# Optimization experiments

Measured on AMD Instinct MI355X. Metric: run time of the kernel, lower is better.

The kernel has to match this reference:

```python
import jax, jax.numpy as jnp
import numpy as np

B, S, D_IN, H, SD = 512, 1024, 64, 64, 4


def setup_inputs() -> dict:
    key = jax.random.key(0)
    ks = jax.random.split(key, 12)
    sc_in = 1.0 / np.sqrt(D_IN)
    sc_h = 1.0 / np.sqrt(H)
    sc_c = 1.0 / np.sqrt(SD + H)
    return {
        "x": jax.random.normal(ks[0], (B, S, D_IN), jnp.float32),
        "W1": jax.random.uniform(ks[1], (H, D_IN), jnp.float32, -sc_in, sc_in),
        "b1": jax.random.uniform(ks[2], (H,), jnp.float32, -sc_in, sc_in),
        "ln_g": jnp.ones((H,), jnp.float32),
        "ln_b": jnp.zeros((H,), jnp.float32),
        "Wi": jax.random.uniform(ks[3], (SD, H), jnp.float32, -sc_h, sc_h),
        "bi": jax.random.uniform(ks[4], (SD,), jnp.float32, -sc_h, sc_h),
        "Wc1": jax.random.uniform(ks[5], (H, SD + H), jnp.float32, -sc_c, sc_c),
        "bc1": jax.random.uniform(ks[6], (H,), jnp.float32, -sc_c, sc_c),
        "Wc2": jax.random.uniform(ks[7], (SD, H), jnp.float32, -sc_h, sc_h),
        "bc2": jax.random.uniform(ks[8], (SD,), jnp.float32, -sc_h, sc_h),
        "corr_scale": jnp.asarray(0.01, jnp.float32),
        "A_level": jnp.zeros((1,), jnp.float32),
        "A_trend": jnp.zeros((1,), jnp.float32),
        "A_gamma": jnp.zeros((1,), jnp.float32),
        "A_resid": jnp.zeros((1,), jnp.float32),
        "omega": jnp.zeros((1,), jnp.float32),
    }


def reference(x, W1, b1, ln_g, ln_b, Wi, bi, Wc1, bc1, Wc2, bc2,
              corr_scale, A_level, A_trend, A_gamma, A_resid, omega):
    # input_proj: Linear -> LayerNorm -> GELU (exact erf), dropout=0
    h = jnp.einsum('bsd,hd->bsh', x, W1) + b1
    mu = jnp.mean(h, axis=-1, keepdims=True)
    var = jnp.mean((h - mu) ** 2, axis=-1, keepdims=True)
    h = (h - mu) * jax.lax.rsqrt(var + 1e-5) * ln_g + ln_b
    h = jax.nn.gelu(h, approximate=False)  # [B,S,H]

    # structured A for state_dim == 4: diag(a_l, a_t, gamma*cos(w), a_r)
    a_l = jax.nn.sigmoid(A_level) * 0.15 + 0.85
    a_t = jax.nn.sigmoid(A_trend) * 0.25 + 0.7
    gamma = jax.nn.sigmoid(A_gamma) * 0.2 + 0.8
    a_r = jax.nn.sigmoid(A_resid) * 0.4
    A = jnp.diag(jnp.concatenate([a_l, a_t, gamma * jnp.cos(omega), a_r]))  # [4,4]

    # innovation applied to all steps at once (batched tiny GEMM)
    bx = jnp.einsum('bsh,kh->bsk', h, Wi) + bi  # [B,S,4]

    def step(s, inp):
        bx_t, h_t = inp  # [B,4], [B,H]
        s_lin = s @ A.T + bx_t
        corr_in = jnp.concatenate([s_lin, h_t], axis=-1)  # [B,4+H]
        c = jax.nn.gelu(corr_in @ Wc1.T + bc1, approximate=False) @ Wc2.T + bc2
        s_new = s_lin + corr_scale * jnp.tanh(c)
        return s_new, s_new

    s0 = jnp.zeros((x.shape[0], SD), x.dtype)
    _, outs = jax.lax.scan(step, s0, (bx.transpose(1, 0, 2), h.transpose(1, 0, 2)))
    return outs.transpose(1, 0, 2)  # [B,S,4] == return_all_states=True
```

## Files before the change

### kernel.cpp

```cpp
#include <hip/hip_runtime.h>
#include <hip/hip_bf16.h>

#define BB 512
#define SS 1024
#define DIN 64
#define HH 64
#define SD4 4
#define CH 64
#define LB 64

typedef __attribute__((ext_vector_type(8))) short s8v;
typedef __attribute__((ext_vector_type(4))) float f4v;

#define MFMA_BF16(a, b, c) __builtin_amdgcn_mfma_f32_16x16x32_bf16((a), (b), (c), 0, 0, 0)

template <int CTRL>
__device__ __forceinline__ float dppf(float v) {
    return __int_as_float(__builtin_amdgcn_mov_dpp(__float_as_int(v), CTRL, 0xF, 0xF, false));
}

__device__ __forceinline__ float rcp_fast(float x) {
    return __builtin_amdgcn_rcpf(x);
}
__device__ __forceinline__ unsigned short f2bf(float f) {
    unsigned int x = __float_as_uint(f);
    x += 0x7fffu + ((x >> 16) & 1u);
    return (unsigned short)(x >> 16);
}
__device__ __forceinline__ float bf2f(unsigned short u) {
    return __uint_as_float(((unsigned int)u) << 16);
}
__device__ __forceinline__ float sigmoid_f(float x) {
    return 1.0f / (1.0f + __expf(-x));
}
__device__ __forceinline__ float tanh_fast(float x) {
    return fmaf(-2.0f, rcp_fast(__expf(2.0f * x) + 1.0f), 1.0f);
}
__device__ __forceinline__ float gelu_fast(float x) {
    float x2 = x * x;
    float z = x * fmaf(x2, -0.0713548162f, -1.5957691216f);
    return x * rcp_fast(1.0f + __expf(z));
}
__device__ __forceinline__ s8v cvt8(const float* __restrict__ p) {
    const float4* q4 = (const float4*)p;
    float4 a = q4[0], b = q4[1];
    s8v r;
    r[0] = (short)f2bf(a.x); r[1] = (short)f2bf(a.y);
    r[2] = (short)f2bf(a.z); r[3] = (short)f2bf(a.w);
    r[4] = (short)f2bf(b.x); r[5] = (short)f2bf(b.y);
    r[6] = (short)f2bf(b.z); r[7] = (short)f2bf(b.w);
    return r;
}

__global__ __launch_bounds__(256)
void prep_mfma(const float* __restrict__ x,
               const float* __restrict__ W1, const float* __restrict__ b1,
               const float* __restrict__ ln_g, const float* __restrict__ ln_b,
               const float* __restrict__ Wi, const float* __restrict__ bi,
               const float* __restrict__ Wc1, const float* __restrict__ bc1,
               uint2* __restrict__ pre4, float* __restrict__ bx)
{
    __shared__ unsigned short xs[4][16 * 80];
    __shared__ unsigned short hb[4][16 * 88];

    const int wave = threadIdx.x >> 6;
    const int lane = threadIdx.x & 63;
    const int c = lane & 15;
    const int q = lane >> 4;
    const int stok = lane >> 4;
    const int skc = lane & 15;

    s8v W1f[4][2], Wc1f[4][2], Wif[2];
#pragma unroll
    for (int n = 0; n < 4; ++n) {
#pragma unroll
        for (int kh = 0; kh < 2; ++kh) {
            W1f[n][kh]  = cvt8(W1  + (4 * c + n) * DIN + q * 8 + kh * 32);
            Wc1f[n][kh] = cvt8(Wc1 + (c + 16 * n) * 68 + 4 + q * 8 + kh * 32);
        }
    }
#pragma unroll
    for (int kh = 0; kh < 2; ++kh) {
        if (c < 4) {
            Wif[kh] = cvt8(Wi + c * HH + q * 8 + kh * 32);
        } else {
            s8v z;
#pragma unroll
            for (int e = 0; e < 8; ++e) z[e] = 0;
            Wif[kh] = z;
        }
    }

    float gln[4], bln[4], b1v[4], bc1v[4];
#pragma unroll
    for (int n = 0; n < 4; ++n) {
        const int j1 = 4 * c + n;
        const int j2 = c + 16 * n;
        gln[n] = ln_g[j1]; bln[n] = ln_b[j1]; b1v[n] = b1[j1];
        bc1v[n] = bc1[j2];
    }
    const float biv = (c < 4) ? bi[c] : 0.0f;

    unsigned short* Xs = xs[wave];
    unsigned short* Hb = hb[wave];
    const long tokW = ((long)blockIdx.x * 4 + wave) * 64;
    const float4* xg = (const float4*)x;

    {
        const long base = tokW * 16;
#pragma unroll
        for (int j = 0; j < 4; ++j) {
            float4 v = xg[base + j * 64 + lane];
            ushort4 u;
            u.x = f2bf(v.x); u.y = f2bf(v.y); u.z = f2bf(v.z); u.w = f2bf(v.w);
            *(ushort4*)(Xs + (j * 4 + stok) * 80 + skc * 4) = u;
        }
    }

#pragma unroll 1
    for (int tile = 0; tile < 4; ++tile) {
        const long tok0 = tokW + tile * 16;

        float4 nx[4];
        if (tile < 3) {
            const long base = (tok0 + 16) * 16;
#pragma unroll
            for (int j = 0; j < 4; ++j) nx[j] = xg[base + j * 64 + lane];
        }

        s8v A0 = *(const s8v*)(Xs + c * 80 + q * 8);
        s8v A1 = *(const s8v*)(Xs + c * 80 + 32 + q * 8);

        f4v acc[4];
#pragma unroll
        for (int n = 0; n < 4; ++n) {
            f4v z = {0.f, 0.f, 0.f, 0.f};
            z = MFMA_BF16(A0, W1f[n][0], z);
            acc[n] = MFMA_BF16(A1, W1f[n][1], z);
        }
#pragma unroll
        for (int n = 0; n < 4; ++n)
#pragma unroll
            for (int r = 0; r < 4; ++r) acc[n][r] += b1v[n];

        float sm[4], sq[4];
#pragma unroll
        for (int r = 0; r < 4; ++r) {
            sm[r] = acc[0][r] + acc[1][r] + acc[2][r] + acc[3][r];
            sq[r] = fmaf(acc[0][r], acc[0][r],
                    fmaf(acc[1][r], acc[1][r],
                    fmaf(acc[2][r], acc[2][r], acc[3][r] * acc[3][r])));
        }
#pragma unroll
        for (int r = 0; r < 4; ++r) { sm[r] += dppf<0x121>(sm[r]); sq[r] += dppf<0x121>(sq[r]); }
#pragma unroll
        for (int r = 0; r < 4; ++r) { sm[r] += dppf<0x122>(sm[r]); sq[r] += dppf<0x122>(sq[r]); }
#pragma unroll
        for (int r = 0; r < 4; ++r) { sm[r] += dppf<0x124>(sm[r]); sq[r] += dppf<0x124>(sq[r]); }
#pragma unroll
        for (int r = 0; r < 4; ++r) { sm[r] += dppf<0x128>(sm[r]); sq[r] += dppf<0x128>(sq[r]); }

#pragma unroll
        for (int r = 0; r < 4; ++r) {
            const float mu = sm[r] * (1.0f / HH);
            const float var = fmaf(-mu, mu, sq[r] * (1.0f / HH));
            const float rstd = rsqrtf(var + 1e-5f);
            const int row = q * 4 + r;
            ushort4 hw;
            {
                float h0 = fmaf((acc[0][r] - mu) * rstd, gln[0], bln[0]);
                float h1 = fmaf((acc[1][r] - mu) * rstd, gln[1], bln[1]);
                float h2 = fmaf((acc[2][r] - mu) * rstd, gln[2], bln[2]);
                float h3 = fmaf((acc[3][r] - mu) * rstd, gln[3], bln[3]);
                hw.x = f2bf(gelu_fast(h0));
                hw.y = f2bf(gelu_fast(h1));
                hw.z = f2bf(gelu_fast(h2));
                hw.w = f2bf(gelu_fast(h3));
            }
            *(ushort4*)(Hb + row * 88 + 4 * c) = hw;
        }

        s8v H0 = *(const s8v*)(Hb + c * 88 + q * 8);
        s8v H1 = *(const s8v*)(Hb + c * 88 + 32 + q * 8);

        f4v p[4];
#pragma unroll
        for (int n = 0; n < 4; ++n) {
            f4v z = {0.f, 0.f, 0.f, 0.f};
            z = MFMA_BF16(H0, Wc1f[n][0], z);
            p[n] = MFMA_BF16(H1, Wc1f[n][1], z);
        }
        f4v bz = {0.f, 0.f, 0.f, 0.f};
        bz = MFMA_BF16(H0, Wif[0], bz);
        bz = MFMA_BF16(H1, Wif[1], bz);

        if (c < 4) {
#pragma unroll
            for (int r = 0; r < 4; ++r)
                bx[(tok0 + q * 4 + r) * SD4 + c] = bz[r] + biv;
        }
#pragma unroll
        for (int r = 0; r < 4; ++r) {
            const long tok = tok0 + q * 4 + r;
            uint2 u;
            u.x = (unsigned int)f2bf(p[0][r] + bc1v[0]) |
                  ((unsigned int)f2bf(p[1][r] + bc1v[1]) << 16);
            u.y = (unsigned int)f2bf(p[2][r] + bc1v[2]) |
                  ((unsigned int)f2bf(p[3][r] + bc1v[3]) << 16);
            pre4[tok * 16 + c] = u;
        }

        if (tile < 3) {
#pragma unroll
            for (int j = 0; j < 4; ++j) {
                ushort4 u;
                u.x = f2bf(nx[j].x); u.y = f2bf(nx[j].y);
                u.z = f2bf(nx[j].z); u.w = f2bf(nx[j].w);
                *(ushort4*)(Xs + (j * 4 + stok) * 80 + skc * 4) = u;
            }
        }
    }
}

__global__ __launch_bounds__(256)
void scan_chunk(const uint2* __restrict__ pre4, const float* __restrict__ bx,
                const float* __restrict__ Wc1, const float* __restrict__ Wc2,
                const float* __restrict__ bc2, const float* __restrict__ corr_scale,
                const float* __restrict__ A_level, const float* __restrict__ A_trend,
                const float* __restrict__ A_gamma, const float* __restrict__ A_resid,
                const float* __restrict__ omega, float* __restrict__ out)
{
    const int tid = threadIdx.x;
    const int task = blockIdx.x * 16 + (tid >> 4);
    const int L = tid & 15;
    const int ci = task >> 9;
    const int b = task & 511;
    const int warm = (ci * CH < LB) ? ci * CH : LB;
    const int t0 = ci * CH - warm;
    const int nsteps = warm + CH;

    float w[4][4], v[4][4];
#pragma unroll
    for (int m = 0; m < 4; ++m) {
        const int j = L + 16 * m;
#pragma unroll
        for (int k = 0; k < 4; ++k) {
            w[m][k] = Wc1[j * 68 + k];
            v[k][m] = Wc2[k * HH + j];
        }
    }
    const float cs = corr_scale[0];
    const float a0 = sigmoid_f(A_level[0]) * 0.15f + 0.85f;
    const float a1 = sigmoid_f(A_trend[0]) * 0.25f + 0.70f;
    const float a2 = (sigmoid_f(A_gamma[0]) * 0.2f + 0.8f) * cosf(omega[0]);
    const float a3 = sigmoid_f(A_resid[0]) * 0.4f;
    const float csel = bc2[L & 3];
    const bool o1 = (L & 1) != 0;
    const bool o2 = (L & 2) != 0;

    const uint2* pp = pre4 + ((long)b * SS + t0) * 16 + L;
    const float4* bp = (const float4*)bx + (long)b * SS + t0;
    float* op = out + ((long)b * SS + t0) * SD4;

    float s0 = 0.f, s1 = 0.f, s2 = 0.f, s3 = 0.f;

    uint2 pv[4]; float4 bv[4];
#pragma unroll
    for (int i = 0; i < 4; ++i) { pv[i] = pp[(long)i * 16]; bv[i] = bp[i]; }

#pragma unroll 2
    for (int tt = 0; tt < nsteps; tt += 4) {
        const int ntt = (tt + 4 < nsteps) ? (tt + 4) : (nsteps - 4);
        const uint2* qp = pp + (long)ntt * 16;
        const float4* qb = bp + ntt;
        uint2 np[4]; float4 nb[4];
#pragma unroll
        for (int i = 0; i < 4; ++i) { np[i] = qp[i * 16]; nb[i] = qb[i]; }

        const bool wr = (tt >= warm);
#pragma unroll
        for (int i = 0; i < 4; ++i) {
            const float l0 = fmaf(a0, s0, bv[i].x);
            const float l1 = fmaf(a1, s1, bv[i].y);
            const float l2 = fmaf(a2, s2, bv[i].z);
            const float l3 = fmaf(a3, s3, bv[i].w);
            const float p0 = bf2f((unsigned short)(pv[i].x & 0xffffu));
            const float p1 = bf2f((unsigned short)(pv[i].x >> 16));
            const float p2 = bf2f((unsigned short)(pv[i].y & 0xffffu));
            const float p3 = bf2f((unsigned short)(pv[i].y >> 16));
            float g[4];
            {
                float ua0 = fmaf(l0, w[0][0], p0), ub0 = fmaf(l2, w[0][2], l3 * w[0][3]);
                float ua1 = fmaf(l0, w[1][0], p1), ub1 = fmaf(l2, w[1][2], l3 * w[1][3]);
                float ua2 = fmaf(l0, w[2][0], p2), ub2 = fmaf(l2, w[2][2], l3 * w[2][3]);
                float ua3 = fmaf(l0, w[3][0], p3), ub3 = fmaf(l2, w[3][2], l3 * w[3][3]);
                g[0] = gelu_fast(fmaf(l1, w[0][1], ua0) + ub0);
                g[1] = gelu_fast(fmaf(l1, w[1][1], ua1) + ub1);
                g[2] = gelu_fast(fmaf(l1, w[2][1], ua2) + ub2);
                g[3] = gelu_fast(fmaf(l1, w[3][1], ua3) + ub3);
            }
            const float P0 = fmaf(g[0], v[0][0], g[1] * v[0][1]) + fmaf(g[2], v[0][2], g[3] * v[0][3]);
            const float P1 = fmaf(g[0], v[1][0], g[1] * v[1][1]) + fmaf(g[2], v[1][2], g[3] * v[1][3]);
            const float P2 = fmaf(g[0], v[2][0], g[1] * v[2][1]) + fmaf(g[2], v[2][2], g[3] * v[2][3]);
            const float P3 = fmaf(g[0], v[3][0], g[1] * v[3][1]) + fmaf(g[2], v[3][2], g[3] * v[3][3]);
            const float k0 = o1 ? P1 : P0, s0s = o1 ? P0 : P1;
            const float k1 = o1 ? P3 : P2, s1s = o1 ? P2 : P3;
            const float Af = k0 + dppf<0xB1>(s0s);
            const float Bf = k1 + dppf<0xB1>(s1s);
            const float kk = o2 ? Bf : Af, ss = o2 ? Af : Bf;
            float T = kk + dppf<0x4E>(ss);
            T += dppf<0x124>(T);
            T += dppf<0x128>(T);
            const float th = tanh_fast(T + csel);
            const float lsel = o2 ? (o1 ? l3 : l2) : (o1 ? l1 : l0);
            const float sval = fmaf(cs, th, lsel);
            s0 = dppf<0x00>(sval);
            s1 = dppf<0x55>(sval);
            s2 = dppf<0xAA>(sval);
            s3 = dppf<0xFF>(sval);
            if (wr && L < 4) op[(tt + i) * SD4 + L] = sval;
        }
#pragma unroll
        for (int i = 0; i < 4; ++i) { pv[i] = np[i]; bv[i] = nb[i]; }
    }
}

extern "C" void kernel_launch(void* const* d_in, const int* in_sizes, int n_in,
                              void* d_out, int out_size, void* d_ws, size_t ws_size,
                              hipStream_t stream) {
    (void)in_sizes; (void)n_in; (void)out_size; (void)ws_size;
    const float* x    = (const float*)d_in[0];
    const float* W1   = (const float*)d_in[1];
    const float* b1   = (const float*)d_in[2];
    const float* ln_g = (const float*)d_in[3];
    const float* ln_b = (const float*)d_in[4];
    const float* Wi   = (const float*)d_in[5];
    const float* bi   = (const float*)d_in[6];
    const float* Wc1  = (const float*)d_in[7];
    const float* bc1  = (const float*)d_in[8];
    const float* Wc2  = (const float*)d_in[9];
    const float* bc2  = (const float*)d_in[10];
    const float* corr = (const float*)d_in[11];
    const float* Al   = (const float*)d_in[12];
    const float* At   = (const float*)d_in[13];
    const float* Ag   = (const float*)d_in[14];
    const float* Ar   = (const float*)d_in[15];
    const float* om   = (const float*)d_in[16];

    uint2* pre4 = (uint2*)d_ws;
    float* bx = (float*)((char*)d_ws + (size_t)BB * SS * 16 * sizeof(uint2));
    float* out = (float*)d_out;

    prep_mfma<<<dim3(2048), dim3(256), 0, stream>>>(
        x, W1, b1, ln_g, ln_b, Wi, bi, Wc1, bc1, pre4, bx);
    scan_chunk<<<dim3(BB * SS / CH / 16), dim3(256), 0, stream>>>(
        pre4, bx, Wc1, Wc2, bc2, corr, Al, At, Ag, Ar, om, out);
}
```

Measured before the change: 301.2 us.

## Software-pipeline prep kernel, load x directly to MFMA fragments, stage Wc1 in LDS

The prep kernel now loads x straight from global memory into MFMA A-fragment registers and converts it with the hardware packed bf16 instruction, removing the LDS staging buffer for x. It computes the first GEMM and LayerNorm for the next tile while the current tile's second GEMM runs, so the two stages overlap. Wc1 fragments move from registers into shared LDS, and biases are folded into the MFMA accumulator init. Launch bounds now request 4 blocks per SM to cut register pressure and raise occupancy. The cost is extra LDS reads per tile and a block-wide sync. v_cvt_pk_bf16_f32 rounding may differ slightly from the manual round-to-nearest-even.

```diff
diff --git a/kernel.cpp b/kernel.cpp
--- a/kernel.cpp
+++ b/kernel.cpp
@@ -22,10 +22,10 @@
 __device__ __forceinline__ float rcp_fast(float x) {
     return __builtin_amdgcn_rcpf(x);
 }
-__device__ __forceinline__ unsigned short f2bf(float f) {
-    unsigned int x = __float_as_uint(f);
-    x += 0x7fffu + ((x >> 16) & 1u);
-    return (unsigned short)(x >> 16);
+__device__ __forceinline__ unsigned int cvt_pk(float lo, float hi) {
+    unsigned int r;
+    asm("v_cvt_pk_bf16_f32 %0, %1, %2" : "=v"(r) : "v"(lo), "v"(hi));
+    return r;
 }
 __device__ __forceinline__ float bf2f(unsigned short u) {
     return __uint_as_float(((unsigned int)u) << 16);
@@ -44,15 +44,13 @@
 __device__ __forceinline__ s8v cvt8(const float* __restrict__ p) {
     const float4* q4 = (const float4*)p;
     float4 a = q4[0], b = q4[1];
-    s8v r;
-    r[0] = (short)f2bf(a.x); r[1] = (short)f2bf(a.y);
-    r[2] = (short)f2bf(a.z); r[3] = (short)f2bf(a.w);
-    r[4] = (short)f2bf(b.x); r[5] = (short)f2bf(b.y);
-    r[6] = (short)f2bf(b.z); r[7] = (short)f2bf(b.w);
-    return r;
-}
-
-__global__ __launch_bounds__(256)
+    union { s8v s; unsigned int u[4]; } r;
+    r.u[0] = cvt_pk(a.x, a.y); r.u[1] = cvt_pk(a.z, a.w);
+    r.u[2] = cvt_pk(b.x, b.y); r.u[3] = cvt_pk(b.z, b.w);
+    return r.s;
+}
+
+__global__ __launch_bounds__(256, 4)
 void prep_mfma(const float* __restrict__ x,
                const float* __restrict__ W1, const float* __restrict__ b1,
                const float* __restrict__ ln_g, const float* __restrict__ ln_b,
@@ -60,25 +58,42 @@
                const float* __restrict__ Wc1, const float* __restrict__ bc1,
                uint2* __restrict__ pre4, float* __restrict__ bx)
 {
-    __shared__ unsigned short xs[4][16 * 80];
     __shared__ unsigned short hb[4][16 * 88];
-
-    const int wave = threadIdx.x >> 6;
-    const int lane = threadIdx.x & 63;
+    __shared__ unsigned short wcs[64 * 72];
+
+    const int tid = threadIdx.x;
+    const int wave = tid >> 6;
+    const int lane = tid & 63;
     const int c = lane & 15;
     const int q = lane >> 4;
-    const int stok = lane >> 4;
-    const int skc = lane & 15;
-
-    s8v W1f[4][2], Wc1f[4][2], Wif[2];
-#pragma unroll
-    for (int n = 0; n < 4; ++n) {
-#pragma unroll
-        for (int kh = 0; kh < 2; ++kh) {
-            W1f[n][kh]  = cvt8(W1  + (4 * c + n) * DIN + q * 8 + kh * 32);
-            Wc1f[n][kh] = cvt8(Wc1 + (c + 16 * n) * 68 + 4 + q * 8 + kh * 32);
-        }
-    }
+
+    const long tokW = ((long)blockIdx.x * 4 + wave) * 64;
+
+    const float* xp = x + (tokW + c) * DIN + q * 8;
+    float4 xf0 = *(const float4*)(xp + 0);
+    float4 xf1 = *(const float4*)(xp + 4);
+    float4 xf2 = *(const float4*)(xp + 32);
+    float4 xf3 = *(const float4*)(xp + 36);
+    xp += 16 * DIN;
+
+    {
+        const int row = tid >> 2, chn = tid & 3;
+        const float4* s4 = (const float4*)(Wc1 + row * 68 + 4 + chn * 16);
+        float4 f0 = s4[0], f1 = s4[1], f2 = s4[2], f3 = s4[3];
+        uint2* dst = (uint2*)(wcs + row * 72 + chn * 16);
+        dst[0] = make_uint2(cvt_pk(f0.x, f0.y), cvt_pk(f0.z, f0.w));
+        dst[1] = make_uint2(cvt_pk(f1.x, f1.y), cvt_pk(f1.z, f1.w));
+        dst[2] = make_uint2(cvt_pk(f2.x, f2.y), cvt_pk(f2.z, f2.w));
+        dst[3] = make_uint2(cvt_pk(f3.x, f3.y), cvt_pk(f3.z, f3.w));
+    }
+    __syncthreads();
+
+    s8v W1f[4][2], Wif[2];
+#pragma unroll
+    for (int n = 0; n < 4; ++n)
+#pragma unroll
+        for (int kh = 0; kh < 2; ++kh)
+            W1f[n][kh] = cvt8(W1 + (4 * c + n) * DIN + q * 8 + kh * 32);
 #pragma unroll
     for (int kh = 0; kh < 2; ++kh) {
         if (c < 4) {
@@ -101,48 +116,18 @@
     }
     const float biv = (c < 4) ? bi[c] : 0.0f;
 
-    unsigned short* Xs = xs[wave];
     unsigned short* Hb = hb[wave];
-    const long tokW = ((long)blockIdx.x * 4 + wave) * 64;
-    const float4* xg = (const float4*)x;
-
-    {
-        const long base = tokW * 16;
-#pragma unroll
-        for (int j = 0; j < 4; ++j) {
-            float4 v = xg[base + j * 64 + lane];
-            ushort4 u;
-            u.x = f2bf(v.x); u.y = f2bf(v.y); u.z = f2bf(v.z); u.w = f2bf(v.w);
-            *(ushort4*)(Xs + (j * 4 + stok) * 80 + skc * 4) = u;
-        }
-    }
-
-#pragma unroll 1
-    for (int tile = 0; tile < 4; ++tile) {
-        const long tok0 = tokW + tile * 16;
-
-        float4 nx[4];
-        if (tile < 3) {
-            const long base = (tok0 + 16) * 16;
-#pragma unroll
-            for (int j = 0; j < 4; ++j) nx[j] = xg[base + j * 64 + lane];
-        }
-
-        s8v A0 = *(const s8v*)(Xs + c * 80 + q * 8);
-        s8v A1 = *(const s8v*)(Xs + c * 80 + 32 + q * 8);
-
+    uint2* pq = pre4 + (tokW + q * 4) * 16 + c;
+    float* bq = bx + (tokW + q * 4) * SD4 + c;
+
+    auto gemm1_ln = [&](s8v A0_, s8v A1_, uint2* hwo) {
         f4v acc[4];
 #pragma unroll
         for (int n = 0; n < 4; ++n) {
-            f4v z = {0.f, 0.f, 0.f, 0.f};
-            z = MFMA_BF16(A0, W1f[n][0], z);
-            acc[n] = MFMA_BF16(A1, W1f[n][1], z);
-        }
-#pragma unroll
-        for (int n = 0; n < 4; ++n)
-#pragma unroll
-            for (int r = 0; r < 4; ++r) acc[n][r] += b1v[n];
-
+            f4v z = { b1v[n], b1v[n], b1v[n], b1v[n] };
+            z = MFMA_BF16(A0_, W1f[n][0], z);
+            acc[n] = MFMA_BF16(A1_, W1f[n][1], z);
+        }
         float sm[4], sq[4];
 #pragma unroll
         for (int r = 0; r < 4; ++r) {
@@ -159,65 +144,90 @@
         for (int r = 0; r < 4; ++r) { sm[r] += dppf<0x124>(sm[r]); sq[r] += dppf<0x124>(sq[r]); }
 #pragma unroll
         for (int r = 0; r < 4; ++r) { sm[r] += dppf<0x128>(sm[r]); sq[r] += dppf<0x128>(sq[r]); }
-
 #pragma unroll
         for (int r = 0; r < 4; ++r) {
             const float mu = sm[r] * (1.0f / HH);
             const float var = fmaf(-mu, mu, sq[r] * (1.0f / HH));
             const float rstd = rsqrtf(var + 1e-5f);
-            const int row = q * 4 + r;
-            ushort4 hw;
-            {
-                float h0 = fmaf((acc[0][r] - mu) * rstd, gln[0], bln[0]);
-                float h1 = fmaf((acc[1][r] - mu) * rstd, gln[1], bln[1]);
-                float h2 = fmaf((acc[2][r] - mu) * rstd, gln[2], bln[2]);
-                float h3 = fmaf((acc[3][r] - mu) * rstd, gln[3], bln[3]);
-                hw.x = f2bf(gelu_fast(h0));
-                hw.y = f2bf(gelu_fast(h1));
-                hw.z = f2bf(gelu_fast(h2));
-                hw.w = f2bf(gelu_fast(h3));
-            }
-            *(ushort4*)(Hb + row * 88 + 4 * c) = hw;
-        }
-
+            float g0 = gelu_fast(fmaf((acc[0][r] - mu) * rstd, gln[0], bln[0]));
+            float g1 = gelu_fast(fmaf((acc[1][r] - mu) * rstd, gln[1], bln[1]));
+            float g2 = gelu_fast(fmaf((acc[2][r] - mu) * rstd, gln[2], bln[2]));
+            float g3 = gelu_fast(fmaf((acc[3][r] - mu) * rstd, gln[3], bln[3]));
+            hwo[r] = make_uint2(cvt_pk(g0, g1), cvt_pk(g2, g3));
+        }
+    };
+
+    s8v A0, A1;
+    {
+        union { s8v s; unsigned int u[4]; } a;
+        a.u[0] = cvt_pk(xf0.x, xf0.y); a.u[1] = cvt_pk(xf0.z, xf0.w);
+        a.u[2] = cvt_pk(xf1.x, xf1.y); a.u[3] = cvt_pk(xf1.z, xf1.w);
+        A0 = a.s;
+        a.u[0] = cvt_pk(xf2.x, xf2.y); a.u[1] = cvt_pk(xf2.z, xf2.w);
+        a.u[2] = cvt_pk(xf3.x, xf3.y); a.u[3] = cvt_pk(xf3.z, xf3.w);
+        A1 = a.s;
+    }
+    xf0 = *(const float4*)(xp + 0);
+    xf1 = *(const float4*)(xp + 4);
+    xf2 = *(const float4*)(xp + 32);
+    xf3 = *(const float4*)(xp + 36);
+    xp += 16 * DIN;
+
+    uint2 hw[4];
+    gemm1_ln(A0, A1, hw);
+#pragma unroll
+    for (int r = 0; r < 4; ++r) *(uint2*)(Hb + (q * 4 + r) * 88 + 4 * c) = hw[r];
+
+#pragma unroll 1
+    for (int t = 0; t < 4; ++t) {
         s8v H0 = *(const s8v*)(Hb + c * 88 + q * 8);
         s8v H1 = *(const s8v*)(Hb + c * 88 + 32 + q * 8);
 
+        uint2 hwn[4];
+        if (t < 3) {
+            union { s8v s; unsigned int u[4]; } a;
+            a.u[0] = cvt_pk(xf0.x, xf0.y); a.u[1] = cvt_pk(xf0.z, xf0.w);
+            a.u[2] = cvt_pk(xf1.x, xf1.y); a.u[3] = cvt_pk(xf1.z, xf1.w);
+            s8v nA0 = a.s;
+            a.u[0] = cvt_pk(xf2.x, xf2.y); a.u[1] = cvt_pk(xf2.z, xf2.w);
+            a.u[2] = cvt_pk(xf3.x, xf3.y); a.u[3] = cvt_pk(xf3.z, xf3.w);
+            s8v nA1 = a.s;
+            if (t < 2) {
+                xf0 = *(const float4*)(xp + 0);
+                xf1 = *(const float4*)(xp + 4);
+                xf2 = *(const float4*)(xp + 32);
+                xf3 = *(const float4*)(xp + 36);
+                xp += 16 * DIN;
+            }
+            gemm1_ln(nA0, nA1, hwn);
+        }
+
         f4v p[4];
 #pragma unroll
         for (int n = 0; n < 4; ++n) {
-            f4v z = {0.f, 0.f, 0.f, 0.f};
-            z = MFMA_BF16(H0, Wc1f[n][0], z);
-            p[n] = MFMA_BF16(H1, Wc1f[n][1], z);
-        }
-        f4v bz = {0.f, 0.f, 0.f, 0.f};
+            const s8v Wf0 = *(const s8v*)(wcs + (c + 16 * n) * 72 + q * 8);
+            const s8v Wf1 = *(const s8v*)(wcs + (c + 16 * n) * 72 + 32 + q * 8);
+            f4v z = { bc1v[n], bc1v[n], bc1v[n], bc1v[n] };
+            z = MFMA_BF16(H0, Wf0, z);
+            p[n] = MFMA_BF16(H1, Wf1, z);
+        }
+        f4v bz = { biv, biv, biv, biv };
         bz = MFMA_BF16(H0, Wif[0], bz);
         bz = MFMA_BF16(H1, Wif[1], bz);
 
         if (c < 4) {
 #pragma unroll
-            for (int r = 0; r < 4; ++r)
-                bx[(tok0 + q * 4 + r) * SD4 + c] = bz[r] + biv;
-        }
-#pragma unroll
-        for (int r = 0; r < 4; ++r) {
-            const long tok = tok0 + q * 4 + r;
-            uint2 u;
-            u.x = (unsigned int)f2bf(p[0][r] + bc1v[0]) |
-                  ((unsigned int)f2bf(p[1][r] + bc1v[1]) << 16);
-            u.y = (unsigned int)f2bf(p[2][r] + bc1v[2]) |
-                  ((unsigned int)f2bf(p[3][r] + bc1v[3]) << 16);
-            pre4[tok * 16 + c] = u;
-        }
-
-        if (tile < 3) {
-#pragma unroll
-            for (int j = 0; j < 4; ++j) {
-                ushort4 u;
-                u.x = f2bf(nx[j].x); u.y = f2bf(nx[j].y);
-                u.z = f2bf(nx[j].z); u.w = f2bf(nx[j].w);
-                *(ushort4*)(Xs + (j * 4 + stok) * 80 + skc * 4) = u;
-            }
+            for (int r = 0; r < 4; ++r) bq[r * SD4] = bz[r];
+        }
+#pragma unroll
+        for (int r = 0; r < 4; ++r)
+            pq[r * 16] = make_uint2(cvt_pk(p[0][r], p[1][r]),
+                                    cvt_pk(p[2][r], p[3][r]));
+        pq += 256; bq += 64;
+
+        if (t < 3) {
+#pragma unroll
+            for (int r = 0; r < 4; ++r) *(uint2*)(Hb + (q * 4 + r) * 88 + 4 * c) = hwn[r];
         }
     }
 }
```

Measured after the change: 323.7 us. 1.07x slower.
